# Kernel tuning notes

Measured on AMD Instinct MI355X. Metric: run time of the kernel, lower is better.

## Reference

```python
import jax, jax.numpy as jnp
import numpy as np

N, E = 50000, 800000          # nodes, edges
IN_CH, HID, HEADS = 256, 32, 4  # conv1: 256 -> 32x4; conv2: 128 -> 128 (1 head)
NEG_SLOPE = 0.2               # PyG GATConv default LeakyReLU slope


def setup_inputs() -> dict:
    key = jax.random.key(0)
    ks = jax.random.split(key, 9)
    H1 = HID * HEADS
    p = lambda k, shape, s: jax.random.normal(k, shape, jnp.float32) * s
    return {
        "x": jax.random.normal(ks[0], (N, IN_CH), jnp.float32),
        "src": jax.random.randint(ks[1], (E,), 0, N, dtype=jnp.int32),
        "dst": jax.random.randint(ks[2], (E,), 0, N, dtype=jnp.int32),
        "W1": p(ks[3], (IN_CH, H1), (2.0 / IN_CH) ** 0.5),
        "att_src1": p(ks[4], (HEADS, HID), 0.1),
        "att_dst1": p(ks[5], (HEADS, HID), 0.1),
        "b1": jnp.zeros((H1,), jnp.float32),
        "W2": p(ks[6], (H1, H1), (2.0 / H1) ** 0.5),
        "att_src2": p(ks[7], (1, H1), 0.1),
        "att_dst2": p(ks[8], (1, H1), 0.1),
        "b2": jnp.zeros((H1,), jnp.float32),
    }


def _gat_conv(x, src, dst, W, a_src, a_dst, b):
    """PyG-style GATConv: project, per-edge attention, segment softmax over dst, scatter-sum."""
    n = x.shape[0]
    H, C = a_src.shape
    xp = (x @ W).reshape(n, H, C)                      # [N,H,C]
    al_s = jnp.sum(xp * a_src, axis=-1)                # [N,H]
    al_d = jnp.sum(xp * a_dst, axis=-1)                # [N,H]
    e = jax.nn.leaky_relu(al_s[src] + al_d[dst], NEG_SLOPE)   # [E,H]
    m = jax.lax.stop_gradient(jax.ops.segment_max(e, dst, num_segments=n))
    ex = jnp.exp(e - m[dst])                           # stable segment softmax
    z = jax.ops.segment_sum(ex, dst, num_segments=n)
    alpha = ex / (z[dst] + 1e-16)                      # [E,H]
    out = jax.ops.segment_sum(xp[src] * alpha[..., None], dst, num_segments=n)
    return out.reshape(n, H * C) + b


def reference(x, src, dst, W1, att_src1, att_dst1, b1, W2, att_src2, att_dst2, b2):
    n = x.shape[0]
    loops = jnp.arange(n, dtype=src.dtype)             # add_self_loops=True (PyG default)
    s = jnp.concatenate([src, loops])
    d = jnp.concatenate([dst, loops])
    # eval mode: dropout is identity
    h = jax.nn.elu(_gat_conv(x, s, d, W1, att_src1, att_dst1, b1))
    return _gat_conv(h, s, d, W2, att_src2, att_dst2, b2)
```

## Files before the change

### kernel.cpp

```cpp
#include <hip/hip_runtime.h>

#define NN 50000
#define NE 800000
#define NEG 0.2f

constexpr int NB1 = (NN + 255) / 256;

__device__ __forceinline__ float lrelu(float x) { return x > 0.f ? x : NEG * x; }

__global__ void hist_k(const int* __restrict__ dst, int* __restrict__ deg) {
    int i = blockIdx.x * 256 + threadIdx.x;
    if (i < NE) atomicAdd(&deg[dst[i]], 1);
}

__global__ void scan1_k(const int* __restrict__ deg, int* __restrict__ roff,
                        int* __restrict__ bsum) {
    __shared__ int s[256];
    int t = threadIdx.x;
    int i = blockIdx.x * 256 + t;
    int v = (i < NN) ? deg[i] : 0;
    s[t] = v; __syncthreads();
    for (int off = 1; off < 256; off <<= 1) {
        int add = (t >= off) ? s[t - off] : 0;
        __syncthreads();
        s[t] += add;
        __syncthreads();
    }
    if (i < NN) roff[i] = s[t] - v;
    if (t == 255) bsum[blockIdx.x] = s[255];
}

__global__ void scan2_k(const int* __restrict__ bsum, int* __restrict__ boff,
                        int* __restrict__ roff) {
    __shared__ int s[256];
    int t = threadIdx.x;
    int v = (t < NB1) ? bsum[t] : 0;
    s[t] = v; __syncthreads();
    for (int off = 1; off < 256; off <<= 1) {
        int add = (t >= off) ? s[t - off] : 0;
        __syncthreads();
        s[t] += add;
        __syncthreads();
    }
    if (t < NB1) boff[t] = s[t] - v;
    if (t == 255) roff[NN] = s[255];
}

__global__ void scan3_k(int* __restrict__ roff, const int* __restrict__ boff,
                        int* __restrict__ cursor) {
    int i = blockIdx.x * 256 + threadIdx.x;
    if (i < NN) {
        int v = roff[i] + boff[blockIdx.x];
        roff[i] = v;
        cursor[i] = v;
    }
}

__global__ void fill_k(const int* __restrict__ src, const int* __restrict__ dst,
                       int* __restrict__ cursor, int* __restrict__ csr) {
    int i = blockIdx.x * 256 + threadIdx.x;
    if (i < NE) {
        int p = atomicAdd(&cursor[dst[i]], 1);
        csr[p] = src[i];
    }
}

template <int K, int HEADS>
__global__ __launch_bounds__(256) void gemm_k(const float* __restrict__ A,
                                              const float* __restrict__ W,
                                              const float* __restrict__ att_s,
                                              const float* __restrict__ att_d,
                                              float* __restrict__ O,
                                              float* __restrict__ als,
                                              float* __restrict__ ald, int M) {
    __shared__ float sAT[32][68];
    __shared__ float sB[32][128];
    int row0 = blockIdx.x * 64;
    int t = threadIdx.x;
    int rg = t >> 5;
    int cg = t & 31;
    float acc[8][4] = {};
    for (int k0 = 0; k0 < K; k0 += 32) {
        #pragma unroll
        for (int p = 0; p < 2; ++p) {
            int r = p * 32 + (t >> 3);
            int kk4 = (t & 7) * 4;
            int gr = row0 + r;
            float4 v = make_float4(0.f, 0.f, 0.f, 0.f);
            if (gr < M) v = *reinterpret_cast<const float4*>(&A[(size_t)gr * K + k0 + kk4]);
            sAT[kk4 + 0][r] = v.x;
            sAT[kk4 + 1][r] = v.y;
            sAT[kk4 + 2][r] = v.z;
            sAT[kk4 + 3][r] = v.w;
        }
        #pragma unroll
        for (int p = 0; p < 4; ++p) {
            int kr = p * 8 + (t >> 5);
            int c4 = (t & 31) * 4;
            *reinterpret_cast<float4*>(&sB[kr][c4]) =
                *reinterpret_cast<const float4*>(&W[(size_t)(k0 + kr) * 128 + c4]);
        }
        __syncthreads();
        #pragma unroll
        for (int kk = 0; kk < 32; ++kk) {
            float4 a0 = *reinterpret_cast<const float4*>(&sAT[kk][rg * 8]);
            float4 a1 = *reinterpret_cast<const float4*>(&sAT[kk][rg * 8 + 4]);
            float4 bv = *reinterpret_cast<const float4*>(&sB[kk][cg * 4]);
            float ar[8] = {a0.x, a0.y, a0.z, a0.w, a1.x, a1.y, a1.z, a1.w};
            #pragma unroll
            for (int r = 0; r < 8; ++r) {
                acc[r][0] += ar[r] * bv.x;
                acc[r][1] += ar[r] * bv.y;
                acc[r][2] += ar[r] * bv.z;
                acc[r][3] += ar[r] * bv.w;
            }
        }
        __syncthreads();
    }
    constexpr int GROUP = 32 / HEADS;
    float4 as4 = *reinterpret_cast<const float4*>(&att_s[cg * 4]);
    float4 ad4 = *reinterpret_cast<const float4*>(&att_d[cg * 4]);
    #pragma unroll
    for (int r = 0; r < 8; ++r) {
        int gr = row0 + rg * 8 + r;
        float4 o = make_float4(acc[r][0], acc[r][1], acc[r][2], acc[r][3]);
        float ps = o.x * as4.x + o.y * as4.y + o.z * as4.z + o.w * as4.w;
        float pd = o.x * ad4.x + o.y * ad4.y + o.z * ad4.z + o.w * ad4.w;
        #pragma unroll
        for (int m = 1; m < GROUP; m <<= 1) {
            ps += __shfl_xor(ps, m, 64);
            pd += __shfl_xor(pd, m, 64);
        }
        if (gr < M) {
            *reinterpret_cast<float4*>(&O[(size_t)gr * 128 + cg * 4]) = o;
            if ((cg & (GROUP - 1)) == 0) {
                int h = cg / GROUP;
                als[(size_t)gr * HEADS + h] = ps;
                ald[(size_t)gr * HEADS + h] = pd;
            }
        }
    }
}

__global__ __launch_bounds__(256) void agg1_k(const int* __restrict__ roff,
                                              const int* __restrict__ csr,
                                              const float* __restrict__ xp,
                                              const float* __restrict__ als,
                                              const float* __restrict__ ald,
                                              const float* __restrict__ b,
                                              float* __restrict__ hout) {
    int node = (blockIdx.x * 256 + threadIdx.x) >> 6;
    int lane = threadIdx.x & 63;
    if (node >= NN) return;
    int hw = lane >> 5;
    int l  = lane & 31;
    int h  = l >> 3;
    int e0 = roff[node], e1 = roff[node + 1];

    float4 adv = *reinterpret_cast<const float4*>(&ald[node * 4]);
    float4 sv  = *reinterpret_cast<const float4*>(&als[node * 4]);
    float adh = (h == 0) ? adv.x : (h == 1) ? adv.y : (h == 2) ? adv.z : adv.w;
    float svh = (h == 0) ? sv.x  : (h == 1) ? sv.y  : (h == 2) ? sv.z  : sv.w;

    float aA0 = 0.f, aA1 = 0.f, aA2 = 0.f, aA3 = 0.f, zA = 0.f;
    float aB0 = 0.f, aB1 = 0.f, aB2 = 0.f, aB3 = 0.f, zB = 0.f;
    if (hw == 0) {
        float ex = __expf(lrelu(svh + adh));
        zA = ex;
        float4 v = *reinterpret_cast<const float4*>(&xp[(size_t)node * 128 + 4 * l]);
        aA0 = ex * v.x; aA1 = ex * v.y; aA2 = ex * v.z; aA3 = ex * v.w;
    }
    for (int j = e0 + hw; j < e1; j += 4) {
        int sA = csr[j];
        int jB = j + 2;
        bool hasB = jB < e1;
        int sB = hasB ? csr[jB] : sA;
        float4 avA = *reinterpret_cast<const float4*>(&als[sA * 4]);
        float4 avB = *reinterpret_cast<const float4*>(&als[sB * 4]);
        float alA = (h == 0) ? avA.x : (h == 1) ? avA.y : (h == 2) ? avA.z : avA.w;
        float alB = (h == 0) ? avB.x : (h == 1) ? avB.y : (h == 2) ? avB.z : avB.w;
        float exA = __expf(lrelu(alA + adh));
        float exB = hasB ? __expf(lrelu(alB + adh)) : 0.f;
        float4 vA = *reinterpret_cast<const float4*>(&xp[(size_t)sA * 128 + 4 * l]);
        float4 vB = *reinterpret_cast<const float4*>(&xp[(size_t)sB * 128 + 4 * l]);
        zA += exA; aA0 += exA * vA.x; aA1 += exA * vA.y; aA2 += exA * vA.z; aA3 += exA * vA.w;
        zB += exB; aB0 += exB * vB.x; aB1 += exB * vB.y; aB2 += exB * vB.z; aB3 += exB * vB.w;
    }
    float a0 = aA0 + aB0, a1 = aA1 + aB1, a2 = aA2 + aB2, a3 = aA3 + aB3, z = zA + zB;
    a0 += __shfl_xor(a0, 32, 64);
    a1 += __shfl_xor(a1, 32, 64);
    a2 += __shfl_xor(a2, 32, 64);
    a3 += __shfl_xor(a3, 32, 64);
    z  += __shfl_xor(z, 32, 64);
    if (hw == 0) {
        float inv = 1.f / (z + 1e-16f);
        float4 bb = *reinterpret_cast<const float4*>(&b[4 * l]);
        float o0 = a0 * inv + bb.x, o1 = a1 * inv + bb.y;
        float o2 = a2 * inv + bb.z, o3 = a3 * inv + bb.w;
        o0 = o0 > 0.f ? o0 : expm1f(o0);
        o1 = o1 > 0.f ? o1 : expm1f(o1);
        o2 = o2 > 0.f ? o2 : expm1f(o2);
        o3 = o3 > 0.f ? o3 : expm1f(o3);
        *reinterpret_cast<float4*>(&hout[(size_t)node * 128 + 4 * l]) =
            make_float4(o0, o1, o2, o3);
    }
}

__global__ __launch_bounds__(256) void agg2_k(const int* __restrict__ roff,
                                              const int* __restrict__ csr,
                                              const float* __restrict__ xp,
                                              const float* __restrict__ als,
                                              const float* __restrict__ ald,
                                              const float* __restrict__ b,
                                              float* __restrict__ out) {
    int node = (blockIdx.x * 256 + threadIdx.x) >> 6;
    int lane = threadIdx.x & 63;
    if (node >= NN) return;
    int hw = lane >> 5;
    int l  = lane & 31;
    int e0 = roff[node], e1 = roff[node + 1];
    float ad = ald[node];
    float sl = als[node];

    float aA0 = 0.f, aA1 = 0.f, aA2 = 0.f, aA3 = 0.f, zA = 0.f;
    float aB0 = 0.f, aB1 = 0.f, aB2 = 0.f, aB3 = 0.f, zB = 0.f;
    if (hw == 0) {
        float ex = __expf(lrelu(sl + ad));
        zA = ex;
        float4 v = *reinterpret_cast<const float4*>(&xp[(size_t)node * 128 + 4 * l]);
        aA0 = ex * v.x; aA1 = ex * v.y; aA2 = ex * v.z; aA3 = ex * v.w;
    }
    for (int j = e0 + hw; j < e1; j += 4) {
        int sA = csr[j];
        int jB = j + 2;
        bool hasB = jB < e1;
        int sB = hasB ? csr[jB] : sA;
        float alA = als[sA];
        float alB = als[sB];
        float exA = __expf(lrelu(alA + ad));
        float exB = hasB ? __expf(lrelu(alB + ad)) : 0.f;
        float4 vA = *reinterpret_cast<const float4*>(&xp[(size_t)sA * 128 + 4 * l]);
        float4 vB = *reinterpret_cast<const float4*>(&xp[(size_t)sB * 128 + 4 * l]);
        zA += exA; aA0 += exA * vA.x; aA1 += exA * vA.y; aA2 += exA * vA.z; aA3 += exA * vA.w;
        zB += exB; aB0 += exB * vB.x; aB1 += exB * vB.y; aB2 += exB * vB.z; aB3 += exB * vB.w;
    }
    float a0 = aA0 + aB0, a1 = aA1 + aB1, a2 = aA2 + aB2, a3 = aA3 + aB3, z = zA + zB;
    a0 += __shfl_xor(a0, 32, 64);
    a1 += __shfl_xor(a1, 32, 64);
    a2 += __shfl_xor(a2, 32, 64);
    a3 += __shfl_xor(a3, 32, 64);
    z  += __shfl_xor(z, 32, 64);
    if (hw == 0) {
        float inv = 1.f / (z + 1e-16f);
        float4 bb = *reinterpret_cast<const float4*>(&b[4 * l]);
        *reinterpret_cast<float4*>(&out[(size_t)node * 128 + 4 * l]) =
            make_float4(a0 * inv + bb.x, a1 * inv + bb.y, a2 * inv + bb.z, a3 * inv + bb.w);
    }
}

extern "C" void kernel_launch(void* const* d_in, const int* in_sizes, int n_in,
                              void* d_out, int out_size, void* d_ws, size_t ws_size,
                              hipStream_t stream) {
    const float* x   = (const float*)d_in[0];
    const int*   src = (const int*)d_in[1];
    const int*   dst = (const int*)d_in[2];
    const float* W1  = (const float*)d_in[3];
    const float* as1 = (const float*)d_in[4];
    const float* ad1 = (const float*)d_in[5];
    const float* b1  = (const float*)d_in[6];
    const float* W2  = (const float*)d_in[7];
    const float* as2 = (const float*)d_in[8];
    const float* ad2 = (const float*)d_in[9];
    const float* b2  = (const float*)d_in[10];
    float* out = (float*)d_out;

    char* ws = (char*)d_ws;
    size_t off = 0;
    auto alloc = [&](size_t bytes) {
        size_t o = off;
        off = (off + bytes + 255) & ~(size_t)255;
        return o;
    };
    int*   roff   = (int*)(ws + alloc((NN + 1) * 4));
    int*   cursor = (int*)(ws + alloc(NN * 4));
    int*   deg    = (int*)(ws + alloc(NN * 4));
    int*   bsum   = (int*)(ws + alloc(256 * 4));
    int*   boff   = (int*)(ws + alloc(256 * 4));
    int*   csr    = (int*)(ws + alloc((size_t)NE * 4));
    float* xp1    = (float*)(ws + alloc((size_t)NN * 128 * 4));
    float* als1   = (float*)(ws + alloc((size_t)NN * 4 * 4));
    float* ald1   = (float*)(ws + alloc((size_t)NN * 4 * 4));
    float* hbuf   = (float*)(ws + alloc((size_t)NN * 128 * 4));
    float* xp2  = xp1;
    float* als2 = als1;
    float* ald2 = ald1;

    hipMemsetAsync(deg, 0, (size_t)NN * 4, stream);
    hist_k<<<(NE + 255) / 256, 256, 0, stream>>>(dst, deg);
    scan1_k<<<NB1, 256, 0, stream>>>(deg, roff, bsum);
    scan2_k<<<1, 256, 0, stream>>>(bsum, boff, roff);
    scan3_k<<<NB1, 256, 0, stream>>>(roff, boff, cursor);
    fill_k<<<(NE + 255) / 256, 256, 0, stream>>>(src, dst, cursor, csr);

    int aggGrid  = (NN + 3) / 4;
    int gemmGrid = (NN + 63) / 64;

    gemm_k<256, 4><<<gemmGrid, 256, 0, stream>>>(x, W1, as1, ad1, xp1, als1, ald1, NN);
    agg1_k<<<aggGrid, 256, 0, stream>>>(roff, csr, xp1, als1, ald1, b1, hbuf);

    gemm_k<128, 1><<<gemmGrid, 256, 0, stream>>>(hbuf, W2, as2, ad2, xp2, als2, ald2, NN);
    agg2_k<<<aggGrid, 256, 0, stream>>>(roff, csr, xp2, als2, ald2, b2, out);
}
```

Measured before the change: 407.0 us.

## Precompute per-edge attention weights in separate kernel before aggregation

Records each CSR slot's destination during fill. A new edge-parallel kernel then computes the unnormalized attention weights exp(leakyrelu(als[src]+ald[dst])) for every edge, and a unified aggregation kernel only gathers those weights and the source features. The aggregation drops max-subtraction and normalizes by the summed weights, unrolled four edges deep across two half-waves. This moves the exp and the scattered als gathers out of the latency-bound aggregation loop. The cost is two extra kernels and extra per-edge weight traffic, and skipping the max-subtraction risks overflow for large logits. A fallback path is kept if the workspace is too small.

```diff
diff --git a/kernel.cpp b/kernel.cpp
--- a/kernel.cpp
+++ b/kernel.cpp
@@ -56,13 +56,41 @@
     }
 }
 
+template <bool WITH_DST>
 __global__ void fill_k(const int* __restrict__ src, const int* __restrict__ dst,
-                       int* __restrict__ cursor, int* __restrict__ csr) {
+                       int* __restrict__ cursor, int* __restrict__ csr,
+                       int* __restrict__ dstOf) {
     int i = blockIdx.x * 256 + threadIdx.x;
     if (i < NE) {
-        int p = atomicAdd(&cursor[dst[i]], 1);
+        int d = dst[i];
+        int p = atomicAdd(&cursor[d], 1);
         csr[p] = src[i];
-    }
+        if (WITH_DST) dstOf[p] = d;
+    }
+}
+
+__global__ void wt1_k(const int* __restrict__ csr, const int* __restrict__ dstOf,
+                      const float* __restrict__ als, const float* __restrict__ ald,
+                      float* __restrict__ w) {
+    int p = blockIdx.x * 256 + threadIdx.x;
+    if (p >= NE) return;
+    int s = csr[p], d = dstOf[p];
+    float4 av = *reinterpret_cast<const float4*>(&als[s * 4]);
+    float4 dv = *reinterpret_cast<const float4*>(&ald[d * 4]);
+    float4 wv;
+    wv.x = __expf(lrelu(av.x + dv.x));
+    wv.y = __expf(lrelu(av.y + dv.y));
+    wv.z = __expf(lrelu(av.z + dv.z));
+    wv.w = __expf(lrelu(av.w + dv.w));
+    *reinterpret_cast<float4*>(&w[(size_t)p * 4]) = wv;
+}
+
+__global__ void wt2_k(const int* __restrict__ csr, const int* __restrict__ dstOf,
+                      const float* __restrict__ als, const float* __restrict__ ald,
+                      float* __restrict__ w) {
+    int p = blockIdx.x * 256 + threadIdx.x;
+    if (p >= NE) return;
+    w[p] = __expf(lrelu(als[csr[p]] + ald[dstOf[p]]));
 }
 
 template <int K, int HEADS>
@@ -142,6 +170,89 @@
     }
 }
 
+template <int HEADS>
+__global__ __launch_bounds__(256) void aggf_k(const int* __restrict__ roff,
+                                              const int* __restrict__ csr,
+                                              const float* __restrict__ w,
+                                              const float* __restrict__ xp,
+                                              const float* __restrict__ als,
+                                              const float* __restrict__ ald,
+                                              const float* __restrict__ b,
+                                              float* __restrict__ outp, int doElu) {
+    int node = (blockIdx.x * 256 + threadIdx.x) >> 6;
+    int lane = threadIdx.x & 63;
+    if (node >= NN) return;
+    int hw = lane >> 5;
+    int l  = lane & 31;
+    int h  = (HEADS == 4) ? (l >> 3) : 0;
+    int e0 = roff[node], e1 = roff[node + 1];
+
+    float selfw;
+    if (HEADS == 4) {
+        float4 adv = *reinterpret_cast<const float4*>(&ald[node * 4]);
+        float4 sv  = *reinterpret_cast<const float4*>(&als[node * 4]);
+        float adh = (h == 0) ? adv.x : (h == 1) ? adv.y : (h == 2) ? adv.z : adv.w;
+        float svh = (h == 0) ? sv.x  : (h == 1) ? sv.y  : (h == 2) ? sv.z  : sv.w;
+        selfw = __expf(lrelu(svh + adh));
+    } else {
+        selfw = __expf(lrelu(als[node] + ald[node]));
+    }
+
+    float aA0 = 0.f, aA1 = 0.f, aA2 = 0.f, aA3 = 0.f, zA = 0.f;
+    float aB0 = 0.f, aB1 = 0.f, aB2 = 0.f, aB3 = 0.f, zB = 0.f;
+    if (hw == 0) {
+        zA = selfw;
+        float4 v = *reinterpret_cast<const float4*>(&xp[(size_t)node * 128 + 4 * l]);
+        aA0 = selfw * v.x; aA1 = selfw * v.y; aA2 = selfw * v.z; aA3 = selfw * v.w;
+    }
+    for (int j = e0 + hw; j < e1; j += 8) {
+        int i1 = j + 2, i2 = j + 4, i3 = j + 6;
+        bool p1 = i1 < e1, p2 = i2 < e1, p3 = i3 < e1;
+        int j1 = p1 ? i1 : j, j2 = p2 ? i2 : j, j3 = p3 ? i3 : j;
+        int s0 = csr[j], s1 = csr[j1], s2 = csr[j2], s3 = csr[j3];
+        float w0, w1v, w2v, w3v;
+        if (HEADS == 4) {
+            w0  = w[(size_t)j  * 4 + h];
+            w1v = w[(size_t)j1 * 4 + h];
+            w2v = w[(size_t)j2 * 4 + h];
+            w3v = w[(size_t)j3 * 4 + h];
+        } else {
+            w0 = w[j]; w1v = w[j1]; w2v = w[j2]; w3v = w[j3];
+        }
+        w1v = p1 ? w1v : 0.f;
+        w2v = p2 ? w2v : 0.f;
+        w3v = p3 ? w3v : 0.f;
+        float4 v0 = *reinterpret_cast<const float4*>(&xp[(size_t)s0 * 128 + 4 * l]);
+        float4 v1 = *reinterpret_cast<const float4*>(&xp[(size_t)s1 * 128 + 4 * l]);
+        float4 v2 = *reinterpret_cast<const float4*>(&xp[(size_t)s2 * 128 + 4 * l]);
+        float4 v3 = *reinterpret_cast<const float4*>(&xp[(size_t)s3 * 128 + 4 * l]);
+        zA += w0;  aA0 += w0 * v0.x;  aA1 += w0 * v0.y;  aA2 += w0 * v0.z;  aA3 += w0 * v0.w;
+        zA += w1v; aA0 += w1v * v1.x; aA1 += w1v * v1.y; aA2 += w1v * v1.z; aA3 += w1v * v1.w;
+        zB += w2v; aB0 += w2v * v2.x; aB1 += w2v * v2.y; aB2 += w2v * v2.z; aB3 += w2v * v2.w;
+        zB += w3v; aB0 += w3v * v3.x; aB1 += w3v * v3.y; aB2 += w3v * v3.z; aB3 += w3v * v3.w;
+    }
+    float a0 = aA0 + aB0, a1 = aA1 + aB1, a2 = aA2 + aB2, a3 = aA3 + aB3, z = zA + zB;
+    a0 += __shfl_xor(a0, 32, 64);
+    a1 += __shfl_xor(a1, 32, 64);
+    a2 += __shfl_xor(a2, 32, 64);
+    a3 += __shfl_xor(a3, 32, 64);
+    z  += __shfl_xor(z, 32, 64);
+    if (hw == 0) {
+        float inv = 1.f / (z + 1e-16f);
+        float4 bb = *reinterpret_cast<const float4*>(&b[4 * l]);
+        float o0 = a0 * inv + bb.x, o1 = a1 * inv + bb.y;
+        float o2 = a2 * inv + bb.z, o3 = a3 * inv + bb.w;
+        if (doElu) {
+            o0 = o0 > 0.f ? o0 : expm1f(o0);
+            o1 = o1 > 0.f ? o1 : expm1f(o1);
+            o2 = o2 > 0.f ? o2 : expm1f(o2);
+            o3 = o3 > 0.f ? o3 : expm1f(o3);
+        }
+        *reinterpret_cast<float4*>(&outp[(size_t)node * 128 + 4 * l]) =
+            make_float4(o0, o1, o2, o3);
+    }
+}
+
 __global__ __launch_bounds__(256) void agg1_k(const int* __restrict__ roff,
                                               const int* __restrict__ csr,
                                               const float* __restrict__ xp,
@@ -291,6 +402,11 @@
     float* als1   = (float*)(ws + alloc((size_t)NN * 4 * 4));
     float* ald1   = (float*)(ws + alloc((size_t)NN * 4 * 4));
     float* hbuf   = (float*)(ws + alloc((size_t)NN * 128 * 4));
+    int*   dstOf  = (int*)(ws + alloc((size_t)NE * 4));
+    float* w1     = (float*)(ws + alloc((size_t)NE * 4 * 4));
+    float* w2     = w1;
+    bool fast = (off <= ws_size);
+
     float* xp2  = xp1;
     float* als2 = als1;
     float* ald2 = ald1;
@@ -300,14 +416,26 @@
     scan1_k<<<NB1, 256, 0, stream>>>(deg, roff, bsum);
     scan2_k<<<1, 256, 0, stream>>>(bsum, boff, roff);
     scan3_k<<<NB1, 256, 0, stream>>>(roff, boff, cursor);
-    fill_k<<<(NE + 255) / 256, 256, 0, stream>>>(src, dst, cursor, csr);
+    int eGrid = (NE + 255) / 256;
+    if (fast) fill_k<true><<<eGrid, 256, 0, stream>>>(src, dst, cursor, csr, dstOf);
+    else      fill_k<false><<<eGrid, 256, 0, stream>>>(src, dst, cursor, csr, dstOf);
 
     int aggGrid  = (NN + 3) / 4;
     int gemmGrid = (NN + 63) / 64;
 
     gemm_k<256, 4><<<gemmGrid, 256, 0, stream>>>(x, W1, as1, ad1, xp1, als1, ald1, NN);
-    agg1_k<<<aggGrid, 256, 0, stream>>>(roff, csr, xp1, als1, ald1, b1, hbuf);
+    if (fast) {
+        wt1_k<<<eGrid, 256, 0, stream>>>(csr, dstOf, als1, ald1, w1);
+        aggf_k<4><<<aggGrid, 256, 0, stream>>>(roff, csr, w1, xp1, als1, ald1, b1, hbuf, 1);
+    } else {
+        agg1_k<<<aggGrid, 256, 0, stream>>>(roff, csr, xp1, als1, ald1, b1, hbuf);
+    }
 
     gemm_k<128, 1><<<gemmGrid, 256, 0, stream>>>(hbuf, W2, as2, ad2, xp2, als2, ald2, NN);
-    agg2_k<<<aggGrid, 256, 0, stream>>>(roff, csr, xp2, als2, ald2, b2, out);
-}
+    if (fast) {
+        wt2_k<<<eGrid, 256, 0, stream>>>(csr, dstOf, als2, ald2, w2);
+        aggf_k<1><<<aggGrid, 256, 0, stream>>>(roff, csr, w2, xp2, als2, ald2, b2, out, 0);
+    } else {
+        agg2_k<<<aggGrid, 256, 0, stream>>>(roff, csr, xp2, als2, ald2, b2, out);
+    }
+}
```

Measured after the change: 408.1 us. No clear change (+0.3%).
